# Kernel tuning notes

Measured on AMD Instinct MI355X. Metric: run time of the kernel, lower is better.

Reference implementation:

```python
import jax, jax.numpy as jnp
import numpy as np

N = 50000          # nodes
E = 1_600_000      # edges (avg degree 32)
D = 128            # in_channels
H = 4              # heads
C = 32             # out_channels per head (H*C == D for residual add)
NEG_SLOPE = 0.2
STEPS = 3


def setup_inputs() -> dict:
    key = jax.random.key(0)
    k1, k2, k3, k4, k5 = jax.random.split(key, 5)
    x = jax.random.normal(k1, (N, D), jnp.float32)
    edge_index = jax.random.randint(k2, (2, E), 0, N)  # row0=src, row1=dst
    W = jax.random.normal(k3, (D, H * C), jnp.float32) * (1.0 / np.sqrt(D))
    a_src = jax.random.normal(k4, (H, C), jnp.float32) * 0.1
    a_dst = jax.random.normal(k5, (H, C), jnp.float32) * 0.1
    return {"x": x, "edge_index": edge_index, "W": W,
            "a_src": a_src, "a_dst": a_dst, "steps": STEPS}


def _attn_conv(x, edge_index, W, a_src, a_dst):
    """One GAT-style attention conv. Returns (out [N,H*C], attn [E,H], logits [E,H])."""
    src, dst = edge_index[0], edge_index[1]
    h = (x @ W).reshape(N, H, C)                      # [N,H,C]
    alpha_src = jnp.einsum('nhc,hc->nh', h, a_src)    # [N,H]
    alpha_dst = jnp.einsum('nhc,hc->nh', h, a_dst)    # [N,H]
    logits = jax.nn.leaky_relu(alpha_src[src] + alpha_dst[dst], NEG_SLOPE)  # [E,H]
    # softmax over incoming edges of each destination node (segment softmax)
    m = jax.ops.segment_max(logits, dst, num_segments=N)      # [N,H]
    m = jnp.where(jnp.isfinite(m), m, 0.0)                    # nodes w/o in-edges
    e = jnp.exp(logits - m[dst])                              # [E,H]
    denom = jax.ops.segment_sum(e, dst, num_segments=N)       # [N,H]
    attn = e / (denom[dst] + 1e-16)                           # [E,H]
    msg = h[src] * attn[..., None]                            # [E,H,C]
    out = jax.ops.segment_sum(msg, dst, num_segments=N)       # [N,H,C]
    return out.reshape(N, H * C), attn, logits


def reference(x, edge_index, W, a_src, a_dst, steps):
    x_s, attn_s, rel_s = [], [], []
    for _ in range(steps):  # fixed small step count, matches the torch Python loop
        x_prime, attn_t, rel_t = _attn_conv(x, edge_index, W, a_src, a_dst)
        x = x + x_prime
        x_s.append(x)
        attn_s.append(attn_t)
        rel_s.append(rel_t)
    return jnp.stack(x_s, 0), jnp.stack(attn_s, 0), jnp.stack(rel_s, 0)
```

## Files before the change

### kernel.cpp

```cpp
#include <hip/hip_runtime.h>
#include <hip/hip_bf16.h>
#include <math.h>

#define NN 50000
#define EE 1600000
#define DD 128
#define HH 4
#define NSTEP 3
#define NEG 0.2f
#define BM 32
#define NPB 8
#define CAPN 128
#define NBUCK 196
#define BUCKCAP 9216
#define P1CH 16384
#define NB1 ((EE + P1CH - 1) / P1CH)

typedef unsigned short ushort8v __attribute__((ext_vector_type(8)));
typedef float float4v __attribute__((ext_vector_type(4)));

__device__ __forceinline__ float leaky(float v) { return v >= 0.0f ? v : NEG * v; }

__device__ __forceinline__ unsigned short bfu(float f) {
    __hip_bfloat16 b = __float2bfloat16(f);
    return *reinterpret_cast<unsigned short*>(&b);
}
__device__ __forceinline__ float ubf(unsigned short u) {
    return __uint_as_float(((unsigned int)u) << 16);
}

__global__ __launch_bounds__(256) void gemm_k2(const float* __restrict__ X,
                                               const float* __restrict__ W,
                                               const float* __restrict__ a_src,
                                               const float* __restrict__ a_dst,
                                               unsigned short* __restrict__ Hb,
                                               float* __restrict__ as_,
                                               float4* __restrict__ nd) {
    __shared__ float xs[BM][132];
    const int tid  = threadIdx.x;
    const int tcol = tid & 31;
    const int trow = tid >> 5;
    const int row0 = blockIdx.x * BM;

    #pragma unroll
    for (int i = 0; i < 4; ++i) {
        const int l  = tid + 256 * i;
        const int r  = l >> 5;
        const int c4 = l & 31;
        float4 v = {0.f, 0.f, 0.f, 0.f};
        if (row0 + r < NN) v = ((const float4*)(X + (size_t)(row0 + r) * DD))[c4];
        *(float4*)&xs[r][c4 * 4] = v;
    }
    __syncthreads();

    const float4* __restrict__ W4 = (const float4*)W;
    float4 acc0 = {0,0,0,0}, acc1 = {0,0,0,0}, acc2 = {0,0,0,0}, acc3 = {0,0,0,0};

    for (int k = 0; k < DD; k += 4) {
        float4 wv0 = W4[(k + 0) * 32 + tcol];
        float4 wv1 = W4[(k + 1) * 32 + tcol];
        float4 wv2 = W4[(k + 2) * 32 + tcol];
        float4 wv3 = W4[(k + 3) * 32 + tcol];
        float4 xv0 = *(const float4*)&xs[4 * trow + 0][k];
        float4 xv1 = *(const float4*)&xs[4 * trow + 1][k];
        float4 xv2 = *(const float4*)&xs[4 * trow + 2][k];
        float4 xv3 = *(const float4*)&xs[4 * trow + 3][k];
        #define GSTEP(ACC, XV) \
            ACC.x += XV.x * wv0.x; ACC.y += XV.x * wv0.y; ACC.z += XV.x * wv0.z; ACC.w += XV.x * wv0.w; \
            ACC.x += XV.y * wv1.x; ACC.y += XV.y * wv1.y; ACC.z += XV.y * wv1.z; ACC.w += XV.y * wv1.w; \
            ACC.x += XV.z * wv2.x; ACC.y += XV.z * wv2.y; ACC.z += XV.z * wv2.z; ACC.w += XV.z * wv2.w; \
            ACC.x += XV.w * wv3.x; ACC.y += XV.w * wv3.y; ACC.z += XV.w * wv3.z; ACC.w += XV.w * wv3.w;
        GSTEP(acc0, xv0) GSTEP(acc1, xv1) GSTEP(acc2, xv2) GSTEP(acc3, xv3)
        #undef GSTEP
    }

    const float4 asv = ((const float4*)a_src)[tcol];
    const float4 adv = ((const float4*)a_dst)[tcol];
    float ps0 = acc0.x*asv.x + acc0.y*asv.y + acc0.z*asv.z + acc0.w*asv.w;
    float ps1 = acc1.x*asv.x + acc1.y*asv.y + acc1.z*asv.z + acc1.w*asv.w;
    float ps2 = acc2.x*asv.x + acc2.y*asv.y + acc2.z*asv.z + acc2.w*asv.w;
    float ps3 = acc3.x*asv.x + acc3.y*asv.y + acc3.z*asv.z + acc3.w*asv.w;
    float pd0 = acc0.x*adv.x + acc0.y*adv.y + acc0.z*adv.z + acc0.w*adv.w;
    float pd1 = acc1.x*adv.x + acc1.y*adv.y + acc1.z*adv.z + acc1.w*adv.w;
    float pd2 = acc2.x*adv.x + acc2.y*adv.y + acc2.z*adv.z + acc2.w*adv.w;
    float pd3 = acc3.x*adv.x + acc3.y*adv.y + acc3.z*adv.z + acc3.w*adv.w;
    #pragma unroll
    for (int off = 1; off < 8; off <<= 1) {
        ps0 += __shfl_xor(ps0, off); ps1 += __shfl_xor(ps1, off);
        ps2 += __shfl_xor(ps2, off); ps3 += __shfl_xor(ps3, off);
        pd0 += __shfl_xor(pd0, off); pd1 += __shfl_xor(pd1, off);
        pd2 += __shfl_xor(pd2, off); pd3 += __shfl_xor(pd3, off);
    }

    #pragma unroll
    for (int i = 0; i < 4; ++i) {
        const int row = row0 + 4 * trow + i;
        if (row >= NN) break;
        const float4 a = (i == 0) ? acc0 : (i == 1) ? acc1 : (i == 2) ? acc2 : acc3;
        ushort4 p;
        p.x = bfu(a.x); p.y = bfu(a.y); p.z = bfu(a.z); p.w = bfu(a.w);
        *(ushort4*)&Hb[(size_t)row * DD + 4 * tcol] = p;
    }
    if ((tcol & 7) == 0) {
        const int head = tcol >> 3;
        #pragma unroll
        for (int i = 0; i < 4; ++i) {
            const int row = row0 + 4 * trow + i;
            if (row >= NN) break;
            const float ps = (i == 0) ? ps0 : (i == 1) ? ps1 : (i == 2) ? ps2 : ps3;
            const float pd = (i == 0) ? pd0 : (i == 1) ? pd1 : (i == 2) ? pd2 : pd3;
            as_[(size_t)row * HH + head] = ps;
            ((float*)(nd + (size_t)row * 3))[head] = pd;
        }
    }
}

__global__ __launch_bounds__(256) void zero_k(int* __restrict__ p, int n) {
    const int i = blockIdx.x * 256 + threadIdx.x;
    if (i < n) p[i] = 0;
}

__global__ __launch_bounds__(256) void p1_k(const int* __restrict__ ei,
                                            int* __restrict__ bcur,
                                            unsigned int* __restrict__ bkeys) {
    __shared__ int hist[NBUCK];
    __shared__ int cur[NBUCK];
    const int tid = threadIdx.x;
    const int e0 = blockIdx.x * P1CH;
    const int e1 = (e0 + P1CH < EE) ? e0 + P1CH : EE;

    for (int i = tid; i < NBUCK; i += 256) hist[i] = 0;
    __syncthreads();
    for (int e = e0 + tid; e < e1; e += 256)
        atomicAdd(&hist[ei[EE + e] >> 8], 1);
    __syncthreads();
    for (int i = tid; i < NBUCK; i += 256)
        cur[i] = (hist[i] > 0) ? atomicAdd(&bcur[i], hist[i]) : 0;
    __syncthreads();
    for (int e = e0 + tid; e < e1; e += 256) {
        const int s = ei[e];
        const int d = ei[EE + e];
        const int b = d >> 8;
        const int pos = atomicAdd(&cur[b], 1);
        if (pos < BUCKCAP)
            bkeys[(size_t)b * BUCKCAP + pos] = ((unsigned int)d << 16) | (unsigned int)s;
    }
}

__global__ __launch_bounds__(256) void p2_k(const int* __restrict__ bcur,
                                            const unsigned int* __restrict__ bkeys,
                                            int* __restrict__ row_start,
                                            int* __restrict__ degA,
                                            unsigned short* __restrict__ csr) {
    __shared__ int hist[256];
    __shared__ int offs[256];
    __shared__ int cur[256];
    const int b = blockIdx.x;
    const int tid = threadIdx.x;
    int ne = bcur[b]; if (ne > BUCKCAP) ne = BUCKCAP;
    const unsigned int* keys = bkeys + (size_t)b * BUCKCAP;

    hist[tid] = 0;
    __syncthreads();
    for (int i = tid; i < ne; i += 256)
        atomicAdd(&hist[(keys[i] >> 16) & 255], 1);
    __syncthreads();
    const int v = hist[tid];
    offs[tid] = v;
    __syncthreads();
    for (int o = 1; o < 256; o <<= 1) {
        const int add = (tid >= o) ? offs[tid - o] : 0;
        __syncthreads();
        offs[tid] += add;
        __syncthreads();
    }
    const int excl = offs[tid] - v;
    const int n = (b << 8) + tid;
    if (n < NN) { row_start[n] = b * BUCKCAP + excl; degA[n] = v; }
    cur[tid] = excl;
    __syncthreads();
    for (int i = tid; i < ne; i += 256) {
        const unsigned int k = keys[i];
        const int local = (int)((k >> 16) & 255);
        const int pos = atomicAdd(&cur[local], 1);
        csr[(size_t)b * BUCKCAP + pos] = (unsigned short)(k & 0xFFFF);
    }
}

__global__ __launch_bounds__(256) void node_k3(const int* __restrict__ row_start,
                                               const int* __restrict__ degA,
                                               const unsigned short* __restrict__ csr,
                                               const float* __restrict__ as_,
                                               float4* __restrict__ nd,
                                               const unsigned short* __restrict__ Hb,
                                               const float* __restrict__ xprev,
                                               float* __restrict__ xout) {
    __shared__ int    src_l[NPB][CAPN];
    __shared__ float4 exp_l[NPB][CAPN];

    const int tid  = threadIdx.x;
    const int nl   = tid >> 5;
    const int lane = tid & 31;
    const int n    = blockIdx.x * NPB + nl;

    int deg = degA[n];
    if (deg > CAPN) deg = CAPN;
    const int row0 = row_start[n];

    if (deg == 0) {
        ((float4*)(xout + (size_t)n * DD))[lane] = ((const float4*)(xprev + (size_t)n * DD))[lane];
        return;
    }

    const float4 adv = nd[(size_t)n * 3];

    float4 mx = {-INFINITY, -INFINITY, -INFINITY, -INFINITY};
    for (int j = lane; j < deg; j += 32) {
        const int s = (int)csr[(size_t)row0 + j];
        const float4 av = *(const float4*)(as_ + (size_t)s * HH);
        float4 l;
        l.x = leaky(av.x + adv.x); l.y = leaky(av.y + adv.y);
        l.z = leaky(av.z + adv.z); l.w = leaky(av.w + adv.w);
        src_l[nl][j] = s; exp_l[nl][j] = l;
        mx.x = fmaxf(mx.x, l.x); mx.y = fmaxf(mx.y, l.y);
        mx.z = fmaxf(mx.z, l.z); mx.w = fmaxf(mx.w, l.w);
    }
    #pragma unroll
    for (int o = 1; o < 32; o <<= 1) {
        mx.x = fmaxf(mx.x, __shfl_xor(mx.x, o));
        mx.y = fmaxf(mx.y, __shfl_xor(mx.y, o));
        mx.z = fmaxf(mx.z, __shfl_xor(mx.z, o));
        mx.w = fmaxf(mx.w, __shfl_xor(mx.w, o));
    }

    float4 ds = {0.f, 0.f, 0.f, 0.f};
    for (int j = lane; j < deg; j += 32) {
        const float4 l = exp_l[nl][j];
        float4 e4;
        e4.x = expf(l.x - mx.x); e4.y = expf(l.y - mx.y);
        e4.z = expf(l.z - mx.z); e4.w = expf(l.w - mx.w);
        exp_l[nl][j] = e4;
        ds.x += e4.x; ds.y += e4.y; ds.z += e4.z; ds.w += e4.w;
    }
    #pragma unroll
    for (int o = 1; o < 32; o <<= 1) {
        ds.x += __shfl_xor(ds.x, o); ds.y += __shfl_xor(ds.y, o);
        ds.z += __shfl_xor(ds.z, o); ds.w += __shfl_xor(ds.w, o);
    }
    float4 inv;
    inv.x = 1.0f / (ds.x + 1e-16f); inv.y = 1.0f / (ds.y + 1e-16f);
    inv.z = 1.0f / (ds.z + 1e-16f); inv.w = 1.0f / (ds.w + 1e-16f);

    if (lane == 0) {
        nd[(size_t)n * 3 + 1] = mx;
        nd[(size_t)n * 3 + 2] = inv;
    }

    const int esel = lane >> 4;
    const int sub  = lane & 15;
    const int hsel = sub >> 2;
    const float invh = (hsel == 0) ? inv.x : (hsel == 1) ? inv.y : (hsel == 2) ? inv.z : inv.w;
    float4 aclo = {0.f, 0.f, 0.f, 0.f};
    float4 achi = {0.f, 0.f, 0.f, 0.f};
    int j0 = 0;
    #pragma unroll 2
    for (; j0 + 2 <= deg; j0 += 2) {
        const int j = j0 + esel;
        const int s = src_l[nl][j];
        const float a = ((const float*)&exp_l[nl][j])[hsel] * invh;
        const ushort8v hv = *(const ushort8v*)&Hb[(size_t)s * DD + 8 * sub];
        aclo.x += ubf(hv[0]) * a; aclo.y += ubf(hv[1]) * a;
        aclo.z += ubf(hv[2]) * a; aclo.w += ubf(hv[3]) * a;
        achi.x += ubf(hv[4]) * a; achi.y += ubf(hv[5]) * a;
        achi.z += ubf(hv[6]) * a; achi.w += ubf(hv[7]) * a;
    }
    if (j0 < deg && esel == 0) {
        const int j = j0;
        const int s = src_l[nl][j];
        const float a = ((const float*)&exp_l[nl][j])[hsel] * invh;
        const ushort8v hv = *(const ushort8v*)&Hb[(size_t)s * DD + 8 * sub];
        aclo.x += ubf(hv[0]) * a; aclo.y += ubf(hv[1]) * a;
        aclo.z += ubf(hv[2]) * a; aclo.w += ubf(hv[3]) * a;
        achi.x += ubf(hv[4]) * a; achi.y += ubf(hv[5]) * a;
        achi.z += ubf(hv[6]) * a; achi.w += ubf(hv[7]) * a;
    }
    aclo.x += __shfl_xor(aclo.x, 16); aclo.y += __shfl_xor(aclo.y, 16);
    aclo.z += __shfl_xor(aclo.z, 16); aclo.w += __shfl_xor(aclo.w, 16);
    achi.x += __shfl_xor(achi.x, 16); achi.y += __shfl_xor(achi.y, 16);
    achi.z += __shfl_xor(achi.z, 16); achi.w += __shfl_xor(achi.w, 16);
    const float4 mine = (esel == 0) ? aclo : achi;
    const int fidx = 2 * sub + esel;
    const float4 xv = ((const float4*)(xprev + (size_t)n * DD))[fidx];
    float4 o;
    o.x = xv.x + mine.x; o.y = xv.y + mine.y; o.z = xv.z + mine.z; o.w = xv.w + mine.w;
    ((float4*)(xout + (size_t)n * DD))[fidx] = o;
}

__global__ __launch_bounds__(256) void edgeattn3_k(const int* __restrict__ ei,
                                                   const float* __restrict__ as3,
                                                   const float4* __restrict__ nd3,
                                                   float* __restrict__ rel_out,
                                                   float* __restrict__ attn_out) {
    const int e = blockIdx.x * 256 + threadIdx.x;
    if (e >= EE) return;
    const int st = blockIdx.y;
    const int s = __builtin_nontemporal_load(ei + e);
    const int d = __builtin_nontemporal_load(ei + EE + e);
    const float4 av = *(const float4*)(as3 + ((size_t)st * NN + s) * HH);
    const float4* ndp = nd3 + ((size_t)st * NN + d) * 3;
    const float4 dv = ndp[0];
    const float4 mm = ndp[1];
    const float4 iv = ndp[2];
    float4v l;
    l.x = leaky(av.x + dv.x); l.y = leaky(av.y + dv.y);
    l.z = leaky(av.z + dv.z); l.w = leaky(av.w + dv.w);
    __builtin_nontemporal_store(l, (float4v*)(rel_out + ((size_t)st * EE + e) * HH));
    float4v a;
    a.x = expf(l.x - mm.x) * iv.x; a.y = expf(l.y - mm.y) * iv.y;
    a.z = expf(l.z - mm.z) * iv.z; a.w = expf(l.w - mm.w) * iv.w;
    __builtin_nontemporal_store(a, (float4v*)(attn_out + ((size_t)st * EE + e) * HH));
}

extern "C" void kernel_launch(void* const* d_in, const int* in_sizes, int n_in,
                              void* d_out, int out_size, void* d_ws, size_t ws_size,
                              hipStream_t stream) {
    const float* x     = (const float*)d_in[0];
    const int*   ei    = (const int*)d_in[1];
    const float* W     = (const float*)d_in[2];
    const float* a_src = (const float*)d_in[3];
    const float* a_dst = (const float*)d_in[4];

    float* xs_out   = (float*)d_out;
    float* attn_out = xs_out + (size_t)NSTEP * NN * DD;
    float* rel_out  = attn_out + (size_t)NSTEP * EE * HH;

    unsigned short* hb = (unsigned short*)d_ws;
    float*  as3   = (float*)(hb + (size_t)NN * DD);
    float4* nd3   = (float4*)(as3 + (size_t)NSTEP * NN * HH);
    int*    bcur  = (int*)(nd3 + (size_t)NSTEP * NN * 3);
    unsigned int* bkeys = (unsigned int*)(bcur + NBUCK);
    int*    rowst = (int*)(bkeys + (size_t)NBUCK * BUCKCAP);
    int*    degA  = rowst + NN;
    unsigned short* csr = (unsigned short*)(degA + NN);

    zero_k<<<1, 256, 0, stream>>>(bcur, NBUCK);
    p1_k<<<NB1, 256, 0, stream>>>(ei, bcur, bkeys);
    p2_k<<<NBUCK, 256, 0, stream>>>(bcur, bkeys, rowst, degA, csr);

    const float* xprev = x;
    for (int s = 0; s < NSTEP; ++s) {
        float* xs_s = xs_out + (size_t)s * NN * DD;
        float* as_  = as3 + (size_t)s * NN * HH;
        float4* nd  = nd3 + (size_t)s * NN * 3;

        gemm_k2<<<(NN + BM - 1) / BM, 256, 0, stream>>>(xprev, W, a_src, a_dst, hb, as_, nd);
        node_k3<<<NN / NPB, 256, 0, stream>>>(rowst, degA, csr, as_, nd, hb, xprev, xs_s);
        xprev = xs_s;
    }
    dim3 eg((EE + 255) / 256, NSTEP);
    edgeattn3_k<<<eg, 256, 0, stream>>>(ei, as3, nd3, rel_out, attn_out);
}
```

Baseline: 477.2 us.

## Split aggregation per head with head-major feature layout for cache locality

Stores the projected features in a head-major layout (four [N,32] slabs) and splits the neighbour aggregation into one pass per head. The first pass computes the softmax and aggregates head 0, writing fp16 normalized weights for heads 1–3 into reused scratch. Three further passes then aggregate one head each. The intent is to make each gathered feature slab small enough to stay cache-resident during the random gathers, at the cost of extra launches, re-reading the CSR, and an fp16 weight round-trip.

```diff
diff --git a/kernel.cpp b/kernel.cpp
--- a/kernel.cpp
+++ b/kernel.cpp
@@ -27,6 +27,12 @@
 }
 __device__ __forceinline__ float ubf(unsigned short u) {
     return __uint_as_float(((unsigned int)u) << 16);
+}
+__device__ __forceinline__ float h2f(unsigned short u) {
+    _Float16 h; __builtin_memcpy(&h, &u, 2); return (float)h;
+}
+__device__ __forceinline__ unsigned short f2h(float f) {
+    _Float16 h = (_Float16)f; unsigned short u; __builtin_memcpy(&u, &h, 2); return u;
 }
 
 __global__ __launch_bounds__(256) void gemm_k2(const float* __restrict__ X,
@@ -92,6 +98,8 @@
         pd2 += __shfl_xor(pd2, off); pd3 += __shfl_xor(pd3, off);
     }
 
+    const int cb = tcol >> 3;
+    const int co = 4 * (tcol & 7);
     #pragma unroll
     for (int i = 0; i < 4; ++i) {
         const int row = row0 + 4 * trow + i;
@@ -99,7 +107,7 @@
         const float4 a = (i == 0) ? acc0 : (i == 1) ? acc1 : (i == 2) ? acc2 : acc3;
         ushort4 p;
         p.x = bfu(a.x); p.y = bfu(a.y); p.z = bfu(a.z); p.w = bfu(a.w);
-        *(ushort4*)&Hb[(size_t)row * DD + 4 * tcol] = p;
+        *(ushort4*)&Hb[((size_t)cb * NN + row) * 32 + co] = p;
     }
     if ((tcol & 7) == 0) {
         const int head = tcol >> 3;
@@ -187,14 +195,18 @@
     }
 }
 
-__global__ __launch_bounds__(256) void node_k3(const int* __restrict__ row_start,
-                                               const int* __restrict__ degA,
-                                               const unsigned short* __restrict__ csr,
-                                               const float* __restrict__ as_,
-                                               float4* __restrict__ nd,
-                                               const unsigned short* __restrict__ Hb,
-                                               const float* __restrict__ xprev,
-                                               float* __restrict__ xout) {
+
+__global__ __launch_bounds__(256) void node_s_k(const int* __restrict__ rowst,
+                                                const int* __restrict__ degA,
+                                                const unsigned short* __restrict__ csr,
+                                                const float* __restrict__ as_,
+                                                float4* __restrict__ nd,
+                                                const unsigned short* __restrict__ Hb0,
+                                                unsigned short* __restrict__ wgt1,
+                                                unsigned short* __restrict__ wgt2,
+                                                unsigned short* __restrict__ wgt3,
+                                                const float* __restrict__ xprev,
+                                                float* __restrict__ xout) {
     __shared__ int    src_l[NPB][CAPN];
     __shared__ float4 exp_l[NPB][CAPN];
 
@@ -205,13 +217,7 @@
 
     int deg = degA[n];
     if (deg > CAPN) deg = CAPN;
-    const int row0 = row_start[n];
-
-    if (deg == 0) {
-        ((float4*)(xout + (size_t)n * DD))[lane] = ((const float4*)(xprev + (size_t)n * DD))[lane];
-        return;
-    }
-
+    const int row0 = rowst[n];
     const float4 adv = nd[(size_t)n * 3];
 
     float4 mx = {-INFINITY, -INFINITY, -INFINITY, -INFINITY};
@@ -256,44 +262,107 @@
         nd[(size_t)n * 3 + 2] = inv;
     }
 
-    const int esel = lane >> 4;
-    const int sub  = lane & 15;
-    const int hsel = sub >> 2;
-    const float invh = (hsel == 0) ? inv.x : (hsel == 1) ? inv.y : (hsel == 2) ? inv.z : inv.w;
-    float4 aclo = {0.f, 0.f, 0.f, 0.f};
-    float4 achi = {0.f, 0.f, 0.f, 0.f};
+    for (int j = lane; j < deg; j += 32) {
+        const float4 e4 = exp_l[nl][j];
+        wgt1[(size_t)row0 + j] = f2h(e4.y * inv.y);
+        wgt2[(size_t)row0 + j] = f2h(e4.z * inv.z);
+        wgt3[(size_t)row0 + j] = f2h(e4.w * inv.w);
+        exp_l[nl][j].x = e4.x * inv.x;
+    }
+
+    const int eq = lane >> 3;
+    const int s8 = lane & 7;
+    float4 acc = {0.f, 0.f, 0.f, 0.f};
     int j0 = 0;
     #pragma unroll 2
-    for (; j0 + 2 <= deg; j0 += 2) {
-        const int j = j0 + esel;
+    for (; j0 + 4 <= deg; j0 += 4) {
+        const int j = j0 + eq;
         const int s = src_l[nl][j];
-        const float a = ((const float*)&exp_l[nl][j])[hsel] * invh;
-        const ushort8v hv = *(const ushort8v*)&Hb[(size_t)s * DD + 8 * sub];
-        aclo.x += ubf(hv[0]) * a; aclo.y += ubf(hv[1]) * a;
-        aclo.z += ubf(hv[2]) * a; aclo.w += ubf(hv[3]) * a;
-        achi.x += ubf(hv[4]) * a; achi.y += ubf(hv[5]) * a;
-        achi.z += ubf(hv[6]) * a; achi.w += ubf(hv[7]) * a;
-    }
-    if (j0 < deg && esel == 0) {
-        const int j = j0;
+        const float w = exp_l[nl][j].x;
+        const ushort4 hv = *(const ushort4*)&Hb0[(size_t)s * 32 + 4 * s8];
+        acc.x += ubf(hv.x) * w; acc.y += ubf(hv.y) * w;
+        acc.z += ubf(hv.z) * w; acc.w += ubf(hv.w) * w;
+    }
+    if (j0 < deg && eq < deg - j0) {
+        const int j = j0 + eq;
         const int s = src_l[nl][j];
-        const float a = ((const float*)&exp_l[nl][j])[hsel] * invh;
-        const ushort8v hv = *(const ushort8v*)&Hb[(size_t)s * DD + 8 * sub];
-        aclo.x += ubf(hv[0]) * a; aclo.y += ubf(hv[1]) * a;
-        aclo.z += ubf(hv[2]) * a; aclo.w += ubf(hv[3]) * a;
-        achi.x += ubf(hv[4]) * a; achi.y += ubf(hv[5]) * a;
-        achi.z += ubf(hv[6]) * a; achi.w += ubf(hv[7]) * a;
-    }
-    aclo.x += __shfl_xor(aclo.x, 16); aclo.y += __shfl_xor(aclo.y, 16);
-    aclo.z += __shfl_xor(aclo.z, 16); aclo.w += __shfl_xor(aclo.w, 16);
-    achi.x += __shfl_xor(achi.x, 16); achi.y += __shfl_xor(achi.y, 16);
-    achi.z += __shfl_xor(achi.z, 16); achi.w += __shfl_xor(achi.w, 16);
-    const float4 mine = (esel == 0) ? aclo : achi;
-    const int fidx = 2 * sub + esel;
-    const float4 xv = ((const float4*)(xprev + (size_t)n * DD))[fidx];
-    float4 o;
-    o.x = xv.x + mine.x; o.y = xv.y + mine.y; o.z = xv.z + mine.z; o.w = xv.w + mine.w;
-    ((float4*)(xout + (size_t)n * DD))[fidx] = o;
+        const float w = exp_l[nl][j].x;
+        const ushort4 hv = *(const ushort4*)&Hb0[(size_t)s * 32 + 4 * s8];
+        acc.x += ubf(hv.x) * w; acc.y += ubf(hv.y) * w;
+        acc.z += ubf(hv.z) * w; acc.w += ubf(hv.w) * w;
+    }
+    acc.x += __shfl_xor(acc.x, 8);  acc.y += __shfl_xor(acc.y, 8);
+    acc.z += __shfl_xor(acc.z, 8);  acc.w += __shfl_xor(acc.w, 8);
+    acc.x += __shfl_xor(acc.x, 16); acc.y += __shfl_xor(acc.y, 16);
+    acc.z += __shfl_xor(acc.z, 16); acc.w += __shfl_xor(acc.w, 16);
+    if (eq == 0) {
+        const float* xp = xprev + (size_t)n * DD + 4 * s8;
+        float*       xo = xout  + (size_t)n * DD + 4 * s8;
+        float4v xv = __builtin_nontemporal_load((const float4v*)xp);
+        float4v o;
+        o.x = xv.x + acc.x; o.y = xv.y + acc.y; o.z = xv.z + acc.z; o.w = xv.w + acc.w;
+        __builtin_nontemporal_store(o, (float4v*)xo);
+    }
+}
+
+__global__ __launch_bounds__(256) void agg_k(const int* __restrict__ rowst,
+                                             const int* __restrict__ degA,
+                                             const unsigned short* __restrict__ csr,
+                                             const unsigned short* __restrict__ wgth,
+                                             const unsigned short* __restrict__ Hbh,
+                                             const float* __restrict__ xprev,
+                                             float* __restrict__ xout,
+                                             int ch0) {
+    __shared__ int   src_l[NPB][CAPN];
+    __shared__ float wgt_l[NPB][CAPN];
+
+    const int tid  = threadIdx.x;
+    const int nl   = tid >> 5;
+    const int lane = tid & 31;
+    const int n    = blockIdx.x * NPB + nl;
+
+    int deg = degA[n];
+    if (deg > CAPN) deg = CAPN;
+    const int row0 = rowst[n];
+
+    for (int j = lane; j < deg; j += 32) {
+        src_l[nl][j] = (int)__builtin_nontemporal_load(csr + (size_t)row0 + j);
+        wgt_l[nl][j] = h2f(__builtin_nontemporal_load(wgth + (size_t)row0 + j));
+    }
+
+    const int eq = lane >> 3;
+    const int s8 = lane & 7;
+    float4 acc = {0.f, 0.f, 0.f, 0.f};
+    int j0 = 0;
+    #pragma unroll 2
+    for (; j0 + 4 <= deg; j0 += 4) {
+        const int j = j0 + eq;
+        const int s = src_l[nl][j];
+        const float w = wgt_l[nl][j];
+        const ushort4 hv = *(const ushort4*)&Hbh[(size_t)s * 32 + 4 * s8];
+        acc.x += ubf(hv.x) * w; acc.y += ubf(hv.y) * w;
+        acc.z += ubf(hv.z) * w; acc.w += ubf(hv.w) * w;
+    }
+    if (j0 < deg && eq < deg - j0) {
+        const int j = j0 + eq;
+        const int s = src_l[nl][j];
+        const float w = wgt_l[nl][j];
+        const ushort4 hv = *(const ushort4*)&Hbh[(size_t)s * 32 + 4 * s8];
+        acc.x += ubf(hv.x) * w; acc.y += ubf(hv.y) * w;
+        acc.z += ubf(hv.z) * w; acc.w += ubf(hv.w) * w;
+    }
+    acc.x += __shfl_xor(acc.x, 8);  acc.y += __shfl_xor(acc.y, 8);
+    acc.z += __shfl_xor(acc.z, 8);  acc.w += __shfl_xor(acc.w, 8);
+    acc.x += __shfl_xor(acc.x, 16); acc.y += __shfl_xor(acc.y, 16);
+    acc.z += __shfl_xor(acc.z, 16); acc.w += __shfl_xor(acc.w, 16);
+    if (eq == 0) {
+        const float* xp = xprev + (size_t)n * DD + ch0 + 4 * s8;
+        float*       xo = xout  + (size_t)n * DD + ch0 + 4 * s8;
+        float4v xv = __builtin_nontemporal_load((const float4v*)xp);
+        float4v o;
+        o.x = xv.x + acc.x; o.y = xv.y + acc.y; o.z = xv.z + acc.z; o.w = xv.w + acc.w;
+        __builtin_nontemporal_store(o, (float4v*)xo);
+    }
 }
 
 __global__ __launch_bounds__(256) void edgeattn3_k(const int* __restrict__ ei,
@@ -334,14 +403,19 @@
     float* attn_out = xs_out + (size_t)NSTEP * NN * DD;
     float* rel_out  = attn_out + (size_t)NSTEP * EE * HH;
 
+    const size_t CSRN = (size_t)NBUCK * BUCKCAP;
+
     unsigned short* hb = (unsigned short*)d_ws;
-    float*  as3   = (float*)(hb + (size_t)NN * DD);
+    float*  as3   = (float*)(hb + (size_t)4 * NN * 32);
     float4* nd3   = (float4*)(as3 + (size_t)NSTEP * NN * HH);
-    int*    bcur  = (int*)(nd3 + (size_t)NSTEP * NN * 3);
-    unsigned int* bkeys = (unsigned int*)(bcur + NBUCK);
-    int*    rowst = (int*)(bkeys + (size_t)NBUCK * BUCKCAP);
+    int*    rowst = (int*)(nd3 + (size_t)NSTEP * NN * 3);
     int*    degA  = rowst + NN;
     unsigned short* csr = (unsigned short*)(degA + NN);
+    int*    bcur  = (int*)(csr + CSRN);
+    unsigned int* bkeys = (unsigned int*)(bcur + NBUCK);
+    unsigned short* wgt1 = (unsigned short*)bkeys;
+    unsigned short* wgt2 = wgt1 + CSRN;
+    unsigned short* wgt3 = wgt2 + CSRN;
 
     zero_k<<<1, 256, 0, stream>>>(bcur, NBUCK);
     p1_k<<<NB1, 256, 0, stream>>>(ei, bcur, bkeys);
@@ -354,7 +428,14 @@
         float4* nd  = nd3 + (size_t)s * NN * 3;
 
         gemm_k2<<<(NN + BM - 1) / BM, 256, 0, stream>>>(xprev, W, a_src, a_dst, hb, as_, nd);
-        node_k3<<<NN / NPB, 256, 0, stream>>>(rowst, degA, csr, as_, nd, hb, xprev, xs_s);
+        node_s_k<<<NN / NPB, 256, 0, stream>>>(rowst, degA, csr, as_, nd, hb,
+                                               wgt1, wgt2, wgt3, xprev, xs_s);
+        agg_k<<<NN / NPB, 256, 0, stream>>>(rowst, degA, csr, wgt1,
+                                            hb + (size_t)1 * NN * 32, xprev, xs_s, 32);
+        agg_k<<<NN / NPB, 256, 0, stream>>>(rowst, degA, csr, wgt2,
+                                            hb + (size_t)2 * NN * 32, xprev, xs_s, 64);
+        agg_k<<<NN / NPB, 256, 0, stream>>>(rowst, degA, csr, wgt3,
+                                            hb + (size_t)3 * NN * 32, xprev, xs_s, 96);
         xprev = xs_s;
     }
     dim3 eg((EE + 255) / 256, NSTEP);
```

After: 572.6 us. 20.0% more time.
